# Optimization experiments

Hardware: AMD Instinct MI355X
Metric: run time of the kernel (lower is better)

The kernel has to match this reference:

```python
import jax, jax.numpy as jnp
import numpy as np

B, S, Y = 4096, 64, 256
H = Y // 2            # hidden_dim = y_dim/2
E = 32                # embed_size
VG, VA = 10000, 2000  # grape / aroma vocab sizes
KG, KA = 8, 20        # ragged slots per sample (0 = padding)
NC, NT = 50, 5        # country_size, tastes_size


def setup_inputs() -> dict:
    key = jax.random.key(0)
    ks = jax.random.split(key, 20)
    w = lambda k, shape: (jax.random.normal(k, shape, dtype=jnp.float32) * 0.02)
    u1 = jax.random.uniform(ks[5], (B, KG), dtype=jnp.float32)
    u2 = jax.random.uniform(ks[6], (B, KG), dtype=jnp.float32)
    grapes_scales = jnp.where(u2 > 0.3, u1 + 0.1, 0.0)
    u3 = jax.random.uniform(ks[7], (B, KA), dtype=jnp.float32)
    u4 = jax.random.uniform(ks[8], (B, KA), dtype=jnp.float32)
    aromas_scales = jnp.where(u4 > 0.3, u3 + 0.1, 0.0)
    return {
        "x_enc": jax.random.normal(ks[0], (B, S, Y), dtype=jnp.float32),
        "grapes": jax.random.randint(ks[1], (B, KG), 0, VG),
        "grapes_scales": grapes_scales,
        "aromas": jax.random.randint(ks[2], (B, KA), 0, VA),
        "aromas_scales": aromas_scales,
        "W_common": w(ks[9], (Y, H)), "b_common": jnp.zeros((H,), jnp.float32),
        "W_country": w(ks[10], (H, NC)), "b_country": jnp.zeros((NC,), jnp.float32),
        "W_type": w(ks[11], (H, 1)), "b_type": jnp.zeros((1,), jnp.float32),
        "W_taste": w(ks[12], (H, NT)), "b_taste": jnp.zeros((NT,), jnp.float32),
        "W_aroma": w(ks[13], (H, E)), "b_aroma": jnp.zeros((E,), jnp.float32),
        "W_grape": w(ks[14], (H, E)), "b_grape": jnp.zeros((E,), jnp.float32),
        "grapes_emb": w(ks[15], (VG, E)),
        "aroma_emb": w(ks[16], (VA, E)),
    }


def reference(x_enc, grapes, grapes_scales, aromas, aromas_scales,
              W_common, b_common, W_country, b_country, W_type, b_type,
              W_taste, b_taste, W_aroma, b_aroma, W_grape, b_grape,
              grapes_emb, aroma_emb):
    # encoder output -> max-pool over sequence dim
    x = jnp.max(x_enc, axis=1)                         # [B, Y]
    y = jax.nn.elu(x @ W_common + b_common)            # [B, H]
    y_country = y @ W_country + b_country              # [B, NC]
    y_type = jax.nn.sigmoid(y @ W_type + b_type)       # [B, 1]
    y_tastes = jax.nn.sigmoid(y @ W_taste + b_taste)   # [B, NT]
    y_grape = y @ W_grape + b_grape                    # [B, E]
    y_aromas = y @ W_aroma + b_aroma                   # [B, E]

    # grapes: score all vocab, gather ragged slots (padded, 0 = pad id)
    pred_g = y_grape @ grapes_emb.T                    # [B, VG]
    mg = (grapes != 0).astype(pred_g.dtype)
    grape_pred = jax.nn.sigmoid(jnp.take_along_axis(pred_g, grapes, axis=1)) * mg
    grape_true = grapes_scales * (grapes_scales != 0).astype(grapes_scales.dtype)

    # aromas: mask is scales != 0
    pred_a = y_aromas @ aroma_emb.T                    # [B, VA]
    ma = (aromas_scales != 0).astype(pred_a.dtype)
    aroma_pred = jax.nn.sigmoid(jnp.take_along_axis(pred_a, aromas, axis=1)) * ma
    aroma_true = aromas_scales * ma

    return (y_country, y_type, y_tastes,
            grape_pred.ravel(), grape_true.ravel(),
            aroma_pred.ravel(), aroma_true.ravel())
```

## Files before the change

kernel.cpp:

```cpp
#include <hip/hip_runtime.h>
#include <stdint.h>

#define B_TOT 4096
#define SEQ   64
#define Y_DIM 256
#define H_DIM 128
#define E_DIM 32
#define KG_N  8
#define KA_N  20
#define NC_N  50
#define NT_N  5

#define ROWS 4
#define NBLK (B_TOT / ROWS)

#define O_COUNTRY 0
#define O_TYPE    (B_TOT * NC_N)
#define O_TASTE   (O_TYPE + B_TOT)
#define O_GPRED   (O_TASTE + B_TOT * NT_N)
#define O_GTRUE   (O_GPRED + B_TOT * KG_N)
#define O_APRED   (O_GTRUE + B_TOT * KG_N)
#define O_ATRUE   (O_APRED + B_TOT * KA_N)

typedef float f4 __attribute__((ext_vector_type(4)));

__device__ __forceinline__ float sigmoidf_(float x) { return 1.0f / (1.0f + __expf(-x)); }

__global__ __launch_bounds__(256) void wine_fused_kernel(
    const float* __restrict__ x_enc,
    const int*   __restrict__ grapes,
    const float* __restrict__ grapes_scales,
    const int*   __restrict__ aromas,
    const float* __restrict__ aromas_scales,
    const float* __restrict__ W_common,
    const float* __restrict__ b_common,
    const float* __restrict__ W_country,
    const float* __restrict__ b_country,
    const float* __restrict__ W_type,
    const float* __restrict__ b_type,
    const float* __restrict__ W_taste,
    const float* __restrict__ b_taste,
    const float* __restrict__ W_aroma,
    const float* __restrict__ b_aroma,
    const float* __restrict__ W_grape,
    const float* __restrict__ b_grape,
    const float* __restrict__ grapes_emb,
    const float* __restrict__ aroma_emb,
    float*       __restrict__ out)
{
    __shared__ float xs[ROWS][Y_DIM];
    __shared__ float ys[ROWS][H_DIM];
    __shared__ float yg[ROWS][E_DIM + 1];
    __shared__ float ya[ROWS][E_DIM + 1];

    const int t  = threadIdx.x;
    const int b0 = blockIdx.x * ROWS;

    {
        const int row = t >> 6;
        const int y0  = (t & 63) * 4;
        const float* xp = x_enc + (size_t)(b0 + row) * SEQ * Y_DIM + y0;
        f4 m = { -3.4e38f, -3.4e38f, -3.4e38f, -3.4e38f };
        #pragma unroll 8
        for (int s = 0; s < SEQ; ++s) {
            f4 a = __builtin_nontemporal_load((const f4*)(xp + (size_t)s * Y_DIM));
            m.x = fmaxf(m.x, a.x); m.y = fmaxf(m.y, a.y);
            m.z = fmaxf(m.z, a.z); m.w = fmaxf(m.w, a.w);
        }
        *(f4*)&xs[row][y0] = m;
    }
    __syncthreads();

    {
        const int row = t >> 6;
        const int h0  = (t & 63) * 2;
        float a0 = 0.f, a1 = 0.f;
        const float* Wp = W_common + h0;
        #pragma unroll 8
        for (int k = 0; k < Y_DIM; ++k) {
            float xv = xs[row][k];
            float2 w = *(const float2*)(Wp + (size_t)k * H_DIM);
            a0 += xv * w.x; a1 += xv * w.y;
        }
        float2 bb = *(const float2*)(b_common + h0);
        a0 += bb.x; a1 += bb.y;
        a0 = (a0 > 0.f) ? a0 : (__expf(a0) - 1.f);
        a1 = (a1 > 0.f) ? a1 : (__expf(a1) - 1.f);
        *(float2*)&ys[row][h0] = make_float2(a0, a1);
    }
    __syncthreads();

    for (int j = t; j < ROWS * 120; j += 256) {
        const int row = j / 120;
        const int c   = j - row * 120;
        const float* Wp;
        int stride;
        if (c < 50)       { Wp = W_country + c;        stride = NC_N;  }
        else if (c == 50) { Wp = W_type;               stride = 1;     }
        else if (c < 56)  { Wp = W_taste + (c - 51);   stride = NT_N;  }
        else if (c < 88)  { Wp = W_grape + (c - 56);   stride = E_DIM; }
        else              { Wp = W_aroma + (c - 88);   stride = E_DIM; }
        float acc = 0.f;
        const float* yv = ys[row];
        #pragma unroll 4
        for (int k = 0; k < H_DIM; ++k)
            acc += yv[k] * Wp[(size_t)k * stride];
        const int b = b0 + row;
        if (c < 50) {
            out[O_COUNTRY + (size_t)b * NC_N + c] = acc + b_country[c];
        } else if (c == 50) {
            out[O_TYPE + b] = sigmoidf_(acc + b_type[0]);
        } else if (c < 56) {
            out[O_TASTE + (size_t)b * NT_N + (c - 51)] = sigmoidf_(acc + b_taste[c - 51]);
        } else if (c < 88) {
            yg[row][c - 56] = acc + b_grape[c - 56];
        } else {
            ya[row][c - 88] = acc + b_aroma[c - 88];
        }
    }
    __syncthreads();

    if (t < ROWS * KG_N) {
        const int row  = t >> 3;
        const int gi   = (b0 + row) * KG_N + (t & 7);
        const int idx  = grapes[gi];
        float pred = 0.f;
        if (idx != 0) {
            const float* ep = grapes_emb + (size_t)idx * E_DIM;
            const float* yv = yg[row];
            float acc = 0.f;
            #pragma unroll
            for (int e = 0; e < E_DIM; e += 4) {
                float4 v = *(const float4*)(ep + e);
                acc += yv[e+0]*v.x + yv[e+1]*v.y + yv[e+2]*v.z + yv[e+3]*v.w;
            }
            pred = sigmoidf_(acc);
        }
        out[O_GPRED + gi] = pred;
        out[O_GTRUE + gi] = grapes_scales[gi];
    } else if (t < ROWS * (KG_N + KA_N)) {
        const int j    = t - ROWS * KG_N;
        const int row  = j / KA_N;
        const int ai   = (b0 + row) * KA_N + (j - row * KA_N);
        const float sc = aromas_scales[ai];
        float pred = 0.f;
        if (sc != 0.f) {
            const int idx = aromas[ai];
            const float* ep = aroma_emb + (size_t)idx * E_DIM;
            const float* yv = ya[row];
            float acc = 0.f;
            #pragma unroll
            for (int e = 0; e < E_DIM; e += 4) {
                float4 v = *(const float4*)(ep + e);
                acc += yv[e+0]*v.x + yv[e+1]*v.y + yv[e+2]*v.z + yv[e+3]*v.w;
            }
            pred = sigmoidf_(acc);
        }
        out[O_APRED + ai] = pred;
        out[O_ATRUE + ai] = sc;
    }
}

extern "C" void kernel_launch(void* const* d_in, const int* in_sizes, int n_in,
                              void* d_out, int out_size, void* d_ws, size_t ws_size,
                              hipStream_t stream) {
    (void)in_sizes; (void)n_in; (void)d_ws; (void)ws_size; (void)out_size;
    const float* x_enc         = (const float*)d_in[0];
    const int*   grapes        = (const int*)  d_in[1];
    const float* grapes_scales = (const float*)d_in[2];
    const int*   aromas        = (const int*)  d_in[3];
    const float* aromas_scales = (const float*)d_in[4];
    const float* W_common      = (const float*)d_in[5];
    const float* b_common      = (const float*)d_in[6];
    const float* W_country     = (const float*)d_in[7];
    const float* b_country     = (const float*)d_in[8];
    const float* W_type        = (const float*)d_in[9];
    const float* b_type        = (const float*)d_in[10];
    const float* W_taste       = (const float*)d_in[11];
    const float* b_taste       = (const float*)d_in[12];
    const float* W_aroma       = (const float*)d_in[13];
    const float* b_aroma       = (const float*)d_in[14];
    const float* W_grape       = (const float*)d_in[15];
    const float* b_grape       = (const float*)d_in[16];
    const float* grapes_emb    = (const float*)d_in[17];
    const float* aroma_emb     = (const float*)d_in[18];
    float* out = (float*)d_out;

    hipLaunchKernelGGL(wine_fused_kernel, dim3(NBLK), dim3(256), 0, stream,
                       x_enc, grapes, grapes_scales, aromas, aromas_scales,
                       W_common, b_common, W_country, b_country, W_type, b_type,
                       W_taste, b_taste, W_aroma, b_aroma, W_grape, b_grape,
                       grapes_emb, aroma_emb, out);
}
```

Measured before the change: 411.7 us.

## Split max-pool into a separate streaming kernel and batch heads over 8 rows

```diff
diff --git a/kernel.cpp b/kernel.cpp
--- a/kernel.cpp
+++ b/kernel.cpp
@@ -11,6 +11,11 @@
 #define NC_N  50
 #define NT_N  5
 
+#define R1   4
+#define NB1  (B_TOT / R1)
+#define R2   8
+#define NB2  (B_TOT / R2)
+
 #define ROWS 4
 #define NBLK (B_TOT / ROWS)
 
@@ -26,24 +31,177 @@
 
 __device__ __forceinline__ float sigmoidf_(float x) { return 1.0f / (1.0f + __expf(-x)); }
 
+__global__ __launch_bounds__(256) void maxpool_k(
+    const float* __restrict__ x_enc, float* __restrict__ xpool)
+{
+    const int t   = threadIdx.x;
+    const int row = blockIdx.x * R1 + (t >> 6);
+    const int y0  = (t & 63) * 4;
+    const float* xp = x_enc + (size_t)row * (SEQ * Y_DIM) + y0;
+    f4 m = { -3.4e38f, -3.4e38f, -3.4e38f, -3.4e38f };
+    #pragma unroll 8
+    for (int s = 0; s < SEQ; ++s) {
+        f4 a = __builtin_nontemporal_load((const f4*)(xp + (size_t)s * Y_DIM));
+        m.x = fmaxf(m.x, a.x); m.y = fmaxf(m.y, a.y);
+        m.z = fmaxf(m.z, a.z); m.w = fmaxf(m.w, a.w);
+    }
+    *(f4*)(xpool + (size_t)row * Y_DIM + y0) = m;
+}
+
+__global__ __launch_bounds__(256) void heads_k(
+    const float* __restrict__ xpool,
+    const int*   __restrict__ grapes,
+    const float* __restrict__ grapes_scales,
+    const int*   __restrict__ aromas,
+    const float* __restrict__ aromas_scales,
+    const float* __restrict__ W_common,  const float* __restrict__ b_common,
+    const float* __restrict__ W_country, const float* __restrict__ b_country,
+    const float* __restrict__ W_type,    const float* __restrict__ b_type,
+    const float* __restrict__ W_taste,   const float* __restrict__ b_taste,
+    const float* __restrict__ W_aroma,   const float* __restrict__ b_aroma,
+    const float* __restrict__ W_grape,   const float* __restrict__ b_grape,
+    const float* __restrict__ grapes_emb,
+    const float* __restrict__ aroma_emb,
+    float*       __restrict__ out)
+{
+    __shared__ float xs[R2][Y_DIM];
+    __shared__ float ys[R2][H_DIM];
+    __shared__ float yg[R2][E_DIM + 1];
+    __shared__ float ya[R2][E_DIM + 1];
+
+    const int t  = threadIdx.x;
+    const int b0 = blockIdx.x * R2;
+
+    {
+        const f4* src = (const f4*)(xpool + (size_t)b0 * Y_DIM);
+        f4* dst = (f4*)xs;
+        #pragma unroll
+        for (int i = 0; i < (R2 * Y_DIM) / (256 * 4); ++i)
+            dst[t + i * 256] = src[t + i * 256];
+    }
+    __syncthreads();
+
+    {
+        const int c  = t & 127;
+        const int r0 = (t >> 7) * 4;
+        float a0 = 0.f, a1 = 0.f, a2 = 0.f, a3 = 0.f;
+        const float* Wp = W_common + c;
+        #pragma unroll 2
+        for (int k = 0; k < Y_DIM; k += 4) {
+            f4 x0 = *(const f4*)&xs[r0 + 0][k];
+            f4 x1 = *(const f4*)&xs[r0 + 1][k];
+            f4 x2 = *(const f4*)&xs[r0 + 2][k];
+            f4 x3 = *(const f4*)&xs[r0 + 3][k];
+            float w0 = Wp[(size_t)(k + 0) * H_DIM];
+            float w1 = Wp[(size_t)(k + 1) * H_DIM];
+            float w2 = Wp[(size_t)(k + 2) * H_DIM];
+            float w3 = Wp[(size_t)(k + 3) * H_DIM];
+            a0 += x0.x * w0; a0 += x0.y * w1; a0 += x0.z * w2; a0 += x0.w * w3;
+            a1 += x1.x * w0; a1 += x1.y * w1; a1 += x1.z * w2; a1 += x1.w * w3;
+            a2 += x2.x * w0; a2 += x2.y * w1; a2 += x2.z * w2; a2 += x2.w * w3;
+            a3 += x3.x * w0; a3 += x3.y * w1; a3 += x3.z * w2; a3 += x3.w * w3;
+        }
+        const float bb = b_common[c];
+        a0 += bb; a1 += bb; a2 += bb; a3 += bb;
+        a0 = (a0 > 0.f) ? a0 : (__expf(a0) - 1.f);
+        a1 = (a1 > 0.f) ? a1 : (__expf(a1) - 1.f);
+        a2 = (a2 > 0.f) ? a2 : (__expf(a2) - 1.f);
+        a3 = (a3 > 0.f) ? a3 : (__expf(a3) - 1.f);
+        ys[r0 + 0][c] = a0;
+        ys[r0 + 1][c] = a1;
+        ys[r0 + 2][c] = a2;
+        ys[r0 + 3][c] = a3;
+    }
+    __syncthreads();
+
+    for (int j = t; j < R2 * 120; j += 256) {
+        const int row = j / 120;
+        const int c   = j - row * 120;
+        const float* Wp;
+        int stride;
+        if (c < 50)       { Wp = W_country + c;        stride = NC_N;  }
+        else if (c == 50) { Wp = W_type;               stride = 1;     }
+        else if (c < 56)  { Wp = W_taste + (c - 51);   stride = NT_N;  }
+        else if (c < 88)  { Wp = W_grape + (c - 56);   stride = E_DIM; }
+        else              { Wp = W_aroma + (c - 88);   stride = E_DIM; }
+        float acc = 0.f;
+        const float* yv = ys[row];
+        #pragma unroll 4
+        for (int k = 0; k < H_DIM; k += 4) {
+            f4 y4 = *(const f4*)&yv[k];
+            acc += y4.x * Wp[(size_t)(k + 0) * stride];
+            acc += y4.y * Wp[(size_t)(k + 1) * stride];
+            acc += y4.z * Wp[(size_t)(k + 2) * stride];
+            acc += y4.w * Wp[(size_t)(k + 3) * stride];
+        }
+        const int b = b0 + row;
+        if (c < 50) {
+            out[O_COUNTRY + (size_t)b * NC_N + c] = acc + b_country[c];
+        } else if (c == 50) {
+            out[O_TYPE + b] = sigmoidf_(acc + b_type[0]);
+        } else if (c < 56) {
+            out[O_TASTE + (size_t)b * NT_N + (c - 51)] = sigmoidf_(acc + b_taste[c - 51]);
+        } else if (c < 88) {
+            yg[row][c - 56] = acc + b_grape[c - 56];
+        } else {
+            ya[row][c - 88] = acc + b_aroma[c - 88];
+        }
+    }
+    __syncthreads();
+
+    if (t < R2 * KG_N) {
+        const int row  = t >> 3;
+        const int gi   = (b0 + row) * KG_N + (t & 7);
+        const int idx  = grapes[gi];
+        float pred = 0.f;
+        if (idx != 0) {
+            const float* ep = grapes_emb + (size_t)idx * E_DIM;
+            const float* yv = yg[row];
+            float acc = 0.f;
+            #pragma unroll
+            for (int e = 0; e < E_DIM; e += 4) {
+                float4 v = *(const float4*)(ep + e);
+                acc += yv[e+0]*v.x + yv[e+1]*v.y + yv[e+2]*v.z + yv[e+3]*v.w;
+            }
+            pred = sigmoidf_(acc);
+        }
+        out[O_GPRED + gi] = pred;
+        out[O_GTRUE + gi] = grapes_scales[gi];
+    } else if (t < R2 * (KG_N + KA_N)) {
+        const int j    = t - R2 * KG_N;
+        const int row  = j / KA_N;
+        const int ai   = (b0 + row) * KA_N + (j - row * KA_N);
+        const float sc = aromas_scales[ai];
+        float pred = 0.f;
+        if (sc != 0.f) {
+            const int idx = aromas[ai];
+            const float* ep = aroma_emb + (size_t)idx * E_DIM;
+            const float* yv = ya[row];
+            float acc = 0.f;
+            #pragma unroll
+            for (int e = 0; e < E_DIM; e += 4) {
+                float4 v = *(const float4*)(ep + e);
+                acc += yv[e+0]*v.x + yv[e+1]*v.y + yv[e+2]*v.z + yv[e+3]*v.w;
+            }
+            pred = sigmoidf_(acc);
+        }
+        out[O_APRED + ai] = pred;
+        out[O_ATRUE + ai] = sc;
+    }
+}
+
 __global__ __launch_bounds__(256) void wine_fused_kernel(
     const float* __restrict__ x_enc,
     const int*   __restrict__ grapes,
     const float* __restrict__ grapes_scales,
     const int*   __restrict__ aromas,
     const float* __restrict__ aromas_scales,
-    const float* __restrict__ W_common,
-    const float* __restrict__ b_common,
-    const float* __restrict__ W_country,
-    const float* __restrict__ b_country,
-    const float* __restrict__ W_type,
-    const float* __restrict__ b_type,
-    const float* __restrict__ W_taste,
-    const float* __restrict__ b_taste,
-    const float* __restrict__ W_aroma,
-    const float* __restrict__ b_aroma,
-    const float* __restrict__ W_grape,
-    const float* __restrict__ b_grape,
+    const float* __restrict__ W_common,  const float* __restrict__ b_common,
+    const float* __restrict__ W_country, const float* __restrict__ b_country,
+    const float* __restrict__ W_type,    const float* __restrict__ b_type,
+    const float* __restrict__ W_taste,   const float* __restrict__ b_taste,
+    const float* __restrict__ W_aroma,   const float* __restrict__ b_aroma,
+    const float* __restrict__ W_grape,   const float* __restrict__ b_grape,
     const float* __restrict__ grapes_emb,
     const float* __restrict__ aroma_emb,
     float*       __restrict__ out)
@@ -164,7 +322,7 @@
 extern "C" void kernel_launch(void* const* d_in, const int* in_sizes, int n_in,
                               void* d_out, int out_size, void* d_ws, size_t ws_size,
                               hipStream_t stream) {
-    (void)in_sizes; (void)n_in; (void)d_ws; (void)ws_size; (void)out_size;
+    (void)in_sizes; (void)n_in; (void)out_size;
     const float* x_enc         = (const float*)d_in[0];
     const int*   grapes        = (const int*)  d_in[1];
     const float* grapes_scales = (const float*)d_in[2];
@@ -186,9 +344,20 @@
     const float* aroma_emb     = (const float*)d_in[18];
     float* out = (float*)d_out;
 
-    hipLaunchKernelGGL(wine_fused_kernel, dim3(NBLK), dim3(256), 0, stream,
-                       x_enc, grapes, grapes_scales, aromas, aromas_scales,
-                       W_common, b_common, W_country, b_country, W_type, b_type,
-                       W_taste, b_taste, W_aroma, b_aroma, W_grape, b_grape,
-                       grapes_emb, aroma_emb, out);
+    const size_t pool_bytes = (size_t)B_TOT * Y_DIM * sizeof(float);
+    if (d_ws != nullptr && ws_size >= pool_bytes) {
+        float* xpool = (float*)d_ws;
+        hipLaunchKernelGGL(maxpool_k, dim3(NB1), dim3(256), 0, stream, x_enc, xpool);
+        hipLaunchKernelGGL(heads_k, dim3(NB2), dim3(256), 0, stream,
+                           xpool, grapes, grapes_scales, aromas, aromas_scales,
+                           W_common, b_common, W_country, b_country, W_type, b_type,
+                           W_taste, b_taste, W_aroma, b_aroma, W_grape, b_grape,
+                           grapes_emb, aroma_emb, out);
+    } else {
+        hipLaunchKernelGGL(wine_fused_kernel, dim3(NBLK), dim3(256), 0, stream,
+                           x_enc, grapes, grapes_scales, aromas, aromas_scales,
+                           W_common, b_common, W_country, b_country, W_type, b_type,
+                           W_taste, b_taste, W_aroma, b_aroma, W_grape, b_grape,
+                           grapes_emb, aroma_emb, out);
+    }
 }
```

Result: no change. 405.8 us (-1.4%).
